# Kernel tuning notes

Measured on AMD Instinct MI355X. Metric: run time of the kernel, lower is better.

## Reference

```python
import jax, jax.numpy as jnp
import numpy as np

EPS = 1e-6
ROPE_BASE = 10000.0


def layer_norm(x, scale, bias):
    mu = jnp.mean(x, axis=-1, keepdims=True)
    var = jnp.mean(jnp.square(x - mu), axis=-1, keepdims=True)
    return (x - mu) * jax.lax.rsqrt(var + EPS) * scale + bias


def make_rope(head_dim, seq_len):
    half = head_dim // 2
    inv_freq = 1.0 / (ROPE_BASE ** (jnp.arange(half, dtype=jnp.float32) / half))
    freqs = jnp.outer(jnp.arange(seq_len, dtype=jnp.float32), inv_freq)  # (T, half)
    cos = jnp.concatenate([jnp.cos(freqs), jnp.cos(freqs)], axis=-1)[:, None, :]  # (T,1,Dh)
    sin = jnp.concatenate([jnp.sin(freqs), jnp.sin(freqs)], axis=-1)[:, None, :]

    def rotate_half(x):
        x1, x2 = x[..., :half], x[..., half:]
        return jnp.concatenate([-x2, x1], axis=-1)

    def apply(q, k):
        return q * cos + rotate_half(q) * sin, k * cos + rotate_half(k) * sin
    return apply


def mha(x, Wq, bq, Wk, bk, Wv, bv, Wo, bo, causal, rope):
    # x: (..., S, D) -> (..., S, D)
    q = jnp.einsum('...sd,dhk->...shk', x, Wq) + bq
    k = jnp.einsum('...sd,dhk->...shk', x, Wk) + bk
    v = jnp.einsum('...sd,dhk->...shk', x, Wv) + bv
    if rope is not None:
        q, k = rope(q, k)
    scale = 1.0 / np.sqrt(q.shape[-1]).astype(np.float32)
    logits = jnp.einsum('...thk,...shk->...hts', q, k) * scale
    if causal:
        S = q.shape[-3]
        mask = jnp.tril(jnp.ones((S, S), dtype=jnp.bool_))
        logits = jnp.where(mask, logits, jnp.finfo(logits.dtype).min)
    probs = jax.nn.softmax(logits, axis=-1)
    o = jnp.einsum('...hts,...shk->...thk', probs, v)
    return jnp.einsum('...thk,hkd->...td', o, Wo) + bo


def setup_inputs() -> dict:
    key = jax.random.key(0)
    B, T, M, D, H, Dh, F = 8, 128, 16, 1024, 16, 64, 4096
    ks = jax.random.split(key, 12)
    s = 0.02
    return {
        'x': jax.random.normal(ks[0], (B, T, M, D), jnp.float32),
        'ln1_scale': jnp.ones((D,), jnp.float32), 'ln1_bias': jnp.zeros((D,), jnp.float32),
        't_Wq': jax.random.normal(ks[1], (D, H, Dh), jnp.float32) * s,
        't_bq': jnp.zeros((H, Dh), jnp.float32),
        't_Wk': jax.random.normal(ks[2], (D, H, Dh), jnp.float32) * s,
        't_bk': jnp.zeros((H, Dh), jnp.float32),
        't_Wv': jax.random.normal(ks[3], (D, H, Dh), jnp.float32) * s,
        't_bv': jnp.zeros((H, Dh), jnp.float32),
        't_Wo': jax.random.normal(ks[4], (H, Dh, D), jnp.float32) * s,
        't_bo': jnp.zeros((D,), jnp.float32),
        'ln2_scale': jnp.ones((D,), jnp.float32), 'ln2_bias': jnp.zeros((D,), jnp.float32),
        'm_Wq': jax.random.normal(ks[5], (D, H, Dh), jnp.float32) * s,
        'm_bq': jnp.zeros((H, Dh), jnp.float32),
        'm_Wk': jax.random.normal(ks[6], (D, H, Dh), jnp.float32) * s,
        'm_bk': jnp.zeros((H, Dh), jnp.float32),
        'm_Wv': jax.random.normal(ks[7], (D, H, Dh), jnp.float32) * s,
        'm_bv': jnp.zeros((H, Dh), jnp.float32),
        'm_Wo': jax.random.normal(ks[8], (H, Dh, D), jnp.float32) * s,
        'm_bo': jnp.zeros((D,), jnp.float32),
        'ln3_scale': jnp.ones((D,), jnp.float32), 'ln3_bias': jnp.zeros((D,), jnp.float32),
        'mlp_W1': jax.random.normal(ks[9], (D, F), jnp.float32) * s,
        'mlp_b1': jnp.zeros((F,), jnp.float32),
        'mlp_W2': jax.random.normal(ks[10], (F, D), jnp.float32) * s,
        'mlp_b2': jnp.zeros((D,), jnp.float32),
    }


def reference(x, ln1_scale, ln1_bias, t_Wq, t_bq, t_Wk, t_bk, t_Wv, t_bv, t_Wo, t_bo,
              ln2_scale, ln2_bias, m_Wq, m_bq, m_Wk, m_bk, m_Wv, m_bv, m_Wo, m_bo,
              ln3_scale, ln3_bias, mlp_W1, mlp_b1, mlp_W2, mlp_b2):
    # x: (B, T, M, D)
    T = x.shape[1]
    Dh = t_Wq.shape[-1]
    rope = make_rope(Dh, T)
    # --- temporal axial attention (causal, RoPE), M folded into batch ---
    h = layer_norm(x, ln1_scale, ln1_bias)
    h = jnp.swapaxes(h, 1, 2)  # (B, M, T, D)
    a = mha(h, t_Wq, t_bq, t_Wk, t_bk, t_Wv, t_bv, t_Wo, t_bo, causal=True, rope=rope)
    x = x + jnp.swapaxes(a, 1, 2)
    # --- modality axial attention (bidirectional, no RoPE), T folded into batch ---
    h = layer_norm(x, ln2_scale, ln2_bias)  # (B, T, M, D), M is seq axis
    x = x + mha(h, m_Wq, m_bq, m_Wk, m_bk, m_Wv, m_bv, m_Wo, m_bo, causal=False, rope=None)
    # --- MLP ---
    h = layer_norm(x, ln3_scale, ln3_bias)
    h = jax.nn.gelu(jnp.einsum('...d,df->...f', h, mlp_W1) + mlp_b1)
    x = x + jnp.einsum('...f,fd->...d', h, mlp_W2) + mlp_b2
    return x
```

## Files before the change

### kernel.cpp

```cpp
#include <hip/hip_runtime.h>
#include <stdint.h>

typedef __attribute__((ext_vector_type(8))) __bf16 bf16x8;
typedef __attribute__((ext_vector_type(4))) float f32x4;

#define DEV static __device__ __forceinline__

DEV unsigned short f2bf(float f) {
    unsigned int u = __float_as_uint(f);
    u = (u + 0x7fffu + ((u >> 16) & 1u)) >> 16;
    return (unsigned short)u;
}
DEV float bf2f(unsigned short h) { return __uint_as_float((unsigned int)h << 16); }

DEV void async_ld16(const void* g, void* l) {
    __builtin_amdgcn_global_load_lds(
        (const __attribute__((address_space(1))) void*)g,
        (__attribute__((address_space(3))) void*)l, 16, 0, 0);
}

DEV f32x4 mfma16(bf16x8 a, bf16x8 b, f32x4 c) {
    return __builtin_amdgcn_mfma_f32_16x16x32_bf16(a, b, c, 0, 0, 0);
}

DEV float gelu_f(float v) {
    float u = 0.7978845608028654f * (v + 0.044715f * v * v * v);
    u = fminf(fmaxf(u, -9.f), 9.f);
    const float e = __expf(2.f * u);
    const float th = (e - 1.f) / (e + 1.f);
    return 0.5f * v * (1.0f + th);
}

__global__ __launch_bounds__(256) void wconv_kernel(
    const float* __restrict__ src, unsigned short* __restrict__ dst, int K, int N)
{
    __shared__ float tile[32][33];
    const int tx = threadIdx.x & 31;
    const int ty = threadIdx.x >> 5;
    const long nb = blockIdx.x;
    const long kb = blockIdx.y;
#pragma unroll
    for (int i = 0; i < 32; i += 8)
        tile[ty + i][tx] = src[(kb * 32 + ty + i) * N + nb * 32 + tx];
    __syncthreads();
#pragma unroll
    for (int i = 0; i < 32; i += 8)
        dst[(nb * 32 + ty + i) * K + kb * 32 + tx] = f2bf(tile[tx][ty + i]);
}

__global__ void pack_bias_kernel(const float* __restrict__ bq, const float* __restrict__ bk,
                                 const float* __restrict__ bv, float* __restrict__ o)
{
    int i = blockIdx.x * 256 + threadIdx.x;
    if (i < 1024) o[i] = bq[i];
    else if (i < 2048) o[i] = bk[i - 1024];
    else if (i < 3072) o[i] = bv[i - 2048];
}

__global__ __launch_bounds__(256) void ln_kernel(
    const float* __restrict__ x, const float* __restrict__ scale,
    const float* __restrict__ bias, unsigned short* __restrict__ out)
{
    const int lane = threadIdx.x & 63;
    const int wave = threadIdx.x >> 6;
    const long tok = (long)blockIdx.x * 4 + wave;
    const float* xp = x + tok * 1024;
    float4 v[4];
    float sum = 0.f, sq = 0.f;
#pragma unroll
    for (int i = 0; i < 4; ++i) {
        v[i] = ((const float4*)xp)[i * 64 + lane];
        sum += v[i].x + v[i].y + v[i].z + v[i].w;
        sq += v[i].x * v[i].x + v[i].y * v[i].y + v[i].z * v[i].z + v[i].w * v[i].w;
    }
#pragma unroll
    for (int off = 1; off < 64; off <<= 1) {
        sum += __shfl_xor(sum, off);
        sq  += __shfl_xor(sq, off);
    }
    const float mu = sum * (1.f / 1024.f);
    const float var = sq * (1.f / 1024.f) - mu * mu;
    const float rs = rsqrtf(var + 1e-6f);
#pragma unroll
    for (int i = 0; i < 4; ++i) {
        const float4 sc = ((const float4*)scale)[i * 64 + lane];
        const float4 bi = ((const float4*)bias)[i * 64 + lane];
        ushort4 o;
        o.x = f2bf((v[i].x - mu) * rs * sc.x + bi.x);
        o.y = f2bf((v[i].y - mu) * rs * sc.y + bi.y);
        o.z = f2bf((v[i].z - mu) * rs * sc.z + bi.z);
        o.w = f2bf((v[i].w - mu) * rs * sc.w + bi.w);
        *(ushort4*)&out[tok * 1024 + (i * 64 + lane) * 4] = o;
    }
}

template <int EPI>
__global__ __launch_bounds__(512, 2) void gemm256_kernel(
    const unsigned short* __restrict__ A, const unsigned short* __restrict__ Bt,
    const float* __restrict__ bias, const float* __restrict__ resid,
    void* __restrict__ Cout, int M, int N, int K, int nbx)
{
    __shared__ __align__(16) unsigned short lds[2][2][16384];
    const int tid = threadIdx.x;
    const int lane = tid & 63;
    const int wave = tid >> 6;
    const int wr = wave >> 2;
    const int wc = wave & 3;
    const int lr = lane & 15;
    const int hi = lane >> 4;

    const int nwg = gridDim.x;
    const int cpx = nwg >> 3;
    int bid = blockIdx.x;
    bid = (bid & 7) * cpx + (bid >> 3);
    const int bx = bid % nbx, by = bid / nbx;
    const long row0 = (long)by * 256;
    const long col0 = (long)bx * 256;

    const int NT = K >> 6;

    const int srow = tid >> 3;
    const int scL = (tid & 7) ^ (srow & 7);
    const unsigned short* gA = A + (row0 + srow) * (long)K + scL * 8;
    const unsigned short* gB = Bt + (col0 + srow) * (long)K + scL * 8;

    auto stage = [&](int kt, int buf) {
        const long ko = (long)kt * 64;
#pragma unroll
        for (int i = 0; i < 4; ++i)
            async_ld16(gA + i * 64 * (long)K + ko, &lds[buf][0][i * 4096 + tid * 8]);
#pragma unroll
        for (int i = 0; i < 4; ++i)
            async_ld16(gB + i * 64 * (long)K + ko, &lds[buf][1][i * 4096 + tid * 8]);
    };

    int cOff[2];
#pragma unroll
    for (int ks = 0; ks < 2; ++ks)
        cOff[ks] = (((ks << 2) | hi) ^ (lr & 7)) << 4;

    f32x4 acc[8][4];
#pragma unroll
    for (int i = 0; i < 8; ++i)
#pragma unroll
        for (int j = 0; j < 4; ++j) acc[i][j] = f32x4{0.f, 0.f, 0.f, 0.f};

    stage(0, 0);
    if (NT > 1) stage(1, 1);

    for (int kt = 0; kt < NT; ++kt) {
        const int cur = kt & 1;
        if (kt == NT - 1) { asm volatile("s_waitcnt vmcnt(0)" ::: "memory"); }
        else              { asm volatile("s_waitcnt vmcnt(8)" ::: "memory"); }
        __builtin_amdgcn_sched_barrier(0);
        __builtin_amdgcn_s_barrier();

        const char* baseA = (const char*)&lds[cur][0][0];
        const char* baseB = (const char*)&lds[cur][1][0];

        bf16x8 bfrag[4][2], afrag[4][2];
#pragma unroll
        for (int n = 0; n < 4; ++n)
#pragma unroll
            for (int ks = 0; ks < 2; ++ks)
                bfrag[n][ks] = *(const bf16x8*)(baseB + (wc * 64 + n * 16 + lr) * 128 + cOff[ks]);
#pragma unroll
        for (int mm = 0; mm < 4; ++mm)
#pragma unroll
            for (int ks = 0; ks < 2; ++ks)
                afrag[mm][ks] = *(const bf16x8*)(baseA + (wr * 128 + mm * 16 + lr) * 128 + cOff[ks]);

        __builtin_amdgcn_s_setprio(1);
#pragma unroll
        for (int ks = 0; ks < 2; ++ks)
#pragma unroll
            for (int mm = 0; mm < 4; ++mm)
#pragma unroll
                for (int n = 0; n < 4; ++n)
                    acc[mm][n] = mfma16(afrag[mm][ks], bfrag[n][ks], acc[mm][n]);
        __builtin_amdgcn_s_setprio(0);

#pragma unroll
        for (int mm = 0; mm < 4; ++mm)
#pragma unroll
            for (int ks = 0; ks < 2; ++ks)
                afrag[mm][ks] = *(const bf16x8*)(baseA + (wr * 128 + 64 + mm * 16 + lr) * 128 + cOff[ks]);

        __builtin_amdgcn_s_setprio(1);
#pragma unroll
        for (int ks = 0; ks < 2; ++ks)
#pragma unroll
            for (int mm = 0; mm < 4; ++mm)
#pragma unroll
                for (int n = 0; n < 4; ++n)
                    acc[4 + mm][n] = mfma16(afrag[mm][ks], bfrag[n][ks], acc[4 + mm][n]);
        __builtin_amdgcn_s_setprio(0);

        __builtin_amdgcn_s_barrier();
        if (kt + 2 < NT) stage(kt + 2, cur);
    }

    float bcol[4];
#pragma unroll
    for (int n = 0; n < 4; ++n) bcol[n] = bias[col0 + wc * 64 + n * 16 + lr];

    if (EPI == 2) {
        float (*eF)[256] = (float (*)[256])&lds[0][0][0];
        float* co = (float*)Cout;
#pragma unroll
        for (int half = 0; half < 2; ++half) {
            if (wr == half) {
#pragma unroll
                for (int m = 0; m < 8; ++m)
#pragma unroll
                    for (int n = 0; n < 4; ++n)
#pragma unroll
                        for (int j = 0; j < 4; ++j)
                            eF[m * 16 + hi * 4 + j][wc * 64 + n * 16 + lr] = acc[m][n][j] + bcol[n];
            }
            __syncthreads();
#pragma unroll
            for (int it = 0; it < 16; ++it) {
                const int idx = it * 512 + tid;
                const int row = idx >> 6;
                const int ch = (idx & 63) * 4;
                const long g = row0 + half * 128 + row;
                float4 v = *(const float4*)&eF[row][ch];
                const float4 rv = *(const float4*)&resid[g * N + col0 + ch];
                v.x += rv.x; v.y += rv.y; v.z += rv.z; v.w += rv.w;
                *(float4*)&co[g * N + col0 + ch] = v;
            }
            __syncthreads();
        }
    } else {
        unsigned short (*eT)[256] = (unsigned short (*)[256])&lds[0][0][0];
        unsigned short* co = (unsigned short*)Cout;
#pragma unroll
        for (int m = 0; m < 8; ++m)
#pragma unroll
            for (int n = 0; n < 4; ++n)
#pragma unroll
                for (int j = 0; j < 4; ++j) {
                    float v = acc[m][n][j] + bcol[n];
                    if (EPI == 1) v = gelu_f(v);
                    eT[wr * 128 + m * 16 + hi * 4 + j][wc * 64 + n * 16 + lr] = f2bf(v);
                }
        __syncthreads();
#pragma unroll
        for (int it = 0; it < 16; ++it) {
            const int idx = it * 512 + tid;
            const int row = idx >> 5;
            const int ch = (idx & 31) * 8;
            *(uint4*)&co[(row0 + row) * N + col0 + ch] = *(const uint4*)&eT[row][ch];
        }
    }
}

__global__ __launch_bounds__(256) void rope_kernel(unsigned short* __restrict__ qkv)
{
    const long tid = (long)blockIdx.x * 256 + threadIdx.x;
    const int d = (int)(tid & 31);
    const int h = (int)((tid >> 5) & 15);
    const int qk = (int)((tid >> 9) & 1);
    const long token = tid >> 10;
    const int t = (int)((token >> 4) & 127);
    unsigned short* p = qkv + token * 3072 + qk * 1024 + h * 64 + d;
    const float x1 = bf2f(p[0]);
    const float x2 = bf2f(p[32]);
    const float inv = __expf((float)d * -0.2878231366242557f);
    const float f = (float)t * inv;
    float sn, cs;
    sincosf(f, &sn, &cs);
    p[0]  = f2bf(x1 * cs - x2 * sn);
    p[32] = f2bf(x2 * cs + x1 * sn);
}

__global__ __launch_bounds__(256) void attn_temporal(
    const unsigned short* __restrict__ qkv, unsigned short* __restrict__ out)
{
    const int bid = blockIdx.x;
    const int h = bid & 15;
    const int mm = (bid >> 4) & 15;
    const int b = bid >> 8;
    const int tid = threadIdx.x;
    const int lane = tid & 63;
    const int wave = tid >> 6;
    const int lr = lane & 15;
    const int lk = (lane >> 4) * 8;
    const int r4 = (lane >> 4) * 4;

    __shared__ __align__(16) unsigned short smemA[128 * 136];
    __shared__ __align__(16) unsigned short smemV[64 * 136];
    unsigned short (*Ks)[72] = (unsigned short (*)[72])smemA;
    unsigned short (*Ps)[136] = (unsigned short (*)[136])smemA;
    unsigned short (*Vt)[136] = (unsigned short (*)[136])smemV;

    const long tokbase = (long)b * 2048 + mm;

#pragma unroll
    for (int i = 0; i < 4; ++i) {
        const int cc = tid + 256 * i;
        const int s = cc >> 3, part = cc & 7;
        const unsigned short* g = qkv + (tokbase + s * 16l) * 3072 + 1024 + h * 64 + part * 8;
        *(uint4*)&Ks[s][part * 8] = *(const uint4*)g;
    }
#pragma unroll
    for (int i = 0; i < 4; ++i) {
        const int cc = tid + 256 * i;
        const int s = cc >> 3, part = cc & 7;
        const unsigned short* g = qkv + (tokbase + s * 16l) * 3072 + 2048 + h * 64 + part * 8;
        union { uint4 u; unsigned short us[8]; } uu;
        uu.u = *(const uint4*)g;
#pragma unroll
        for (int j = 0; j < 8; ++j) Vt[part * 8 + j][s] = uu.us[j];
    }
    __syncthreads();

    bf16x8 qf[2][2];
#pragma unroll
    for (int rb = 0; rb < 2; ++rb)
#pragma unroll
        for (int ks = 0; ks < 2; ++ks) {
            const int t = wave * 32 + rb * 16 + lr;
            qf[rb][ks] = *(const bf16x8*)(qkv + (tokbase + t * 16l) * 3072 + h * 64 + ks * 32 + lk);
        }

    f32x4 sacc[2][8];
#pragma unroll
    for (int rb = 0; rb < 2; ++rb)
#pragma unroll
        for (int cb = 0; cb < 8; ++cb) sacc[rb][cb] = f32x4{0.f, 0.f, 0.f, 0.f};

#pragma unroll
    for (int cb = 0; cb < 8; ++cb)
#pragma unroll
        for (int ks = 0; ks < 2; ++ks) {
            const bf16x8 kf = *(const bf16x8*)&Ks[cb * 16 + lr][ks * 32 + lk];
            sacc[0][cb] = mfma16(qf[0][ks], kf, sacc[0][cb]);
            sacc[1][cb] = mfma16(qf[1][ks], kf, sacc[1][cb]);
        }

    float recip[2][4];
#pragma unroll
    for (int rb = 0; rb < 2; ++rb)
#pragma unroll
        for (int r = 0; r < 4; ++r) {
            const int trow = wave * 32 + rb * 16 + r4 + r;
            float mx = -1e30f;
#pragma unroll
            for (int cb = 0; cb < 8; ++cb) {
                const int s = cb * 16 + lr;
                const float v = (s <= trow) ? sacc[rb][cb][r] * 0.125f : -1e30f;
                sacc[rb][cb][r] = v;
                mx = fmaxf(mx, v);
            }
            mx = fmaxf(mx, __shfl_xor(mx, 1));
            mx = fmaxf(mx, __shfl_xor(mx, 2));
            mx = fmaxf(mx, __shfl_xor(mx, 4));
            mx = fmaxf(mx, __shfl_xor(mx, 8));
            float sum = 0.f;
#pragma unroll
            for (int cb = 0; cb < 8; ++cb) {
                const float e = __expf(sacc[rb][cb][r] - mx);
                sacc[rb][cb][r] = e;
                sum += e;
            }
            sum += __shfl_xor(sum, 1);
            sum += __shfl_xor(sum, 2);
            sum += __shfl_xor(sum, 4);
            sum += __shfl_xor(sum, 8);
            recip[rb][r] = 1.f / sum;
        }
    __syncthreads();

#pragma unroll
    for (int rb = 0; rb < 2; ++rb)
#pragma unroll
        for (int cb = 0; cb < 8; ++cb)
#pragma unroll
            for (int r = 0; r < 4; ++r)
                Ps[wave * 32 + rb * 16 + r4 + r][cb * 16 + lr] = f2bf(sacc[rb][cb][r]);
    __syncthreads();

    f32x4 oacc[2][4];
#pragma unroll
    for (int rb = 0; rb < 2; ++rb)
#pragma unroll
        for (int cb = 0; cb < 4; ++cb) oacc[rb][cb] = f32x4{0.f, 0.f, 0.f, 0.f};

#pragma unroll
    for (int ks = 0; ks < 4; ++ks) {
        bf16x8 pf[2];
        pf[0] = *(const bf16x8*)&Ps[wave * 32 + lr][ks * 32 + lk];
        pf[1] = *(const bf16x8*)&Ps[wave * 32 + 16 + lr][ks * 32 + lk];
#pragma unroll
        for (int cb = 0; cb < 4; ++cb) {
            const bf16x8 vf = *(const bf16x8*)&Vt[cb * 16 + lr][ks * 32 + lk];
            oacc[0][cb] = mfma16(pf[0], vf, oacc[0][cb]);
            oacc[1][cb] = mfma16(pf[1], vf, oacc[1][cb]);
        }
    }

#pragma unroll
    for (int rb = 0; rb < 2; ++rb)
#pragma unroll
        for (int cb = 0; cb < 4; ++cb)
#pragma unroll
            for (int r = 0; r < 4; ++r) {
                const int trow = wave * 32 + rb * 16 + r4 + r;
                out[(tokbase + trow * 16l) * 1024 + h * 64 + cb * 16 + lr] =
                    f2bf(oacc[rb][cb][r] * recip[rb][r]);
            }
}

__global__ __launch_bounds__(256) void attn_modality(
    const unsigned short* __restrict__ qkv, unsigned short* __restrict__ out)
{
    const int tid = threadIdx.x;
    const int lane = tid & 63;
    const int wave = tid >> 6;
    const int lr = lane & 15;
    const int lk = (lane >> 4) * 8;
    const int r4 = (lane >> 4) * 4;
    const long base = (long)blockIdx.x * 16;

    __shared__ __align__(16) unsigned short smem[4][64 * 40 + 16 * 40];
    unsigned short (*Vt)[40] = (unsigned short (*)[40]) & smem[wave][0];
    unsigned short (*Pl)[40] = (unsigned short (*)[40]) & smem[wave][64 * 40];

    for (int i = lane; i < 400; i += 64)
        *(uint4*)&smem[wave][i * 8] = make_uint4(0u, 0u, 0u, 0u);

    for (int hi = 0; hi < 4; ++hi) {
        const int h = wave * 4 + hi;
#pragma unroll
        for (int i = 0; i < 2; ++i) {
            const int cc = lane + 64 * i;
            const int s = cc >> 3, d0 = (cc & 7) * 8;
            union { uint4 u; unsigned short us[8]; } uu;
            uu.u = *(const uint4*)(qkv + (base + s) * 3072 + 2048 + h * 64 + d0);
#pragma unroll
            for (int j = 0; j < 8; ++j) Vt[d0 + j][s] = uu.us[j];
        }
        bf16x8 qf[2], kf[2];
#pragma unroll
        for (int ks = 0; ks < 2; ++ks) {
            qf[ks] = *(const bf16x8*)(qkv + (base + lr) * 3072 + h * 64 + ks * 32 + lk);
            kf[ks] = *(const bf16x8*)(qkv + (base + lr) * 3072 + 1024 + h * 64 + ks * 32 + lk);
        }
        f32x4 sv = f32x4{0.f, 0.f, 0.f, 0.f};
        sv = mfma16(qf[0], kf[0], sv);
        sv = mfma16(qf[1], kf[1], sv);

        float recip[4], pe[4];
#pragma unroll
        for (int r = 0; r < 4; ++r) {
            const float v = sv[r] * 0.125f;
            float mx = v;
            mx = fmaxf(mx, __shfl_xor(mx, 1));
            mx = fmaxf(mx, __shfl_xor(mx, 2));
            mx = fmaxf(mx, __shfl_xor(mx, 4));
            mx = fmaxf(mx, __shfl_xor(mx, 8));
            const float e = __expf(v - mx);
            float sum = e;
            sum += __shfl_xor(sum, 1);
            sum += __shfl_xor(sum, 2);
            sum += __shfl_xor(sum, 4);
            sum += __shfl_xor(sum, 8);
            recip[r] = 1.f / sum;
            pe[r] = e;
        }
#pragma unroll
        for (int r = 0; r < 4; ++r) Pl[r4 + r][lr] = f2bf(pe[r]);

        const bf16x8 pf = *(const bf16x8*)&Pl[lr][lk];
#pragma unroll
        for (int cb = 0; cb < 4; ++cb) {
            const bf16x8 vf = *(const bf16x8*)&Vt[cb * 16 + lr][lk];
            f32x4 o = f32x4{0.f, 0.f, 0.f, 0.f};
            o = mfma16(pf, vf, o);
#pragma unroll
            for (int r = 0; r < 4; ++r)
                out[(base + r4 + r) * 1024 + h * 64 + cb * 16 + lr] = f2bf(o[r] * recip[r]);
        }
    }
}

extern "C" void kernel_launch(void* const* d_in, const int* in_sizes, int n_in,
                              void* d_out, int out_size, void* d_ws, size_t ws_size,
                              hipStream_t stream)
{
    (void)in_sizes; (void)n_in; (void)out_size;
    const float* x    = (const float*)d_in[0];
    const float* ln1s = (const float*)d_in[1];
    const float* ln1b = (const float*)d_in[2];
    const float* tWq  = (const float*)d_in[3];
    const float* tbq  = (const float*)d_in[4];
    const float* tWk  = (const float*)d_in[5];
    const float* tbk  = (const float*)d_in[6];
    const float* tWv  = (const float*)d_in[7];
    const float* tbv  = (const float*)d_in[8];
    const float* tWo  = (const float*)d_in[9];
    const float* tbo  = (const float*)d_in[10];
    const float* ln2s = (const float*)d_in[11];
    const float* ln2b = (const float*)d_in[12];
    const float* mWq  = (const float*)d_in[13];
    const float* mbq  = (const float*)d_in[14];
    const float* mWk  = (const float*)d_in[15];
    const float* mbk  = (const float*)d_in[16];
    const float* mWv  = (const float*)d_in[17];
    const float* mbv  = (const float*)d_in[18];
    const float* mWo  = (const float*)d_in[19];
    const float* mbo  = (const float*)d_in[20];
    const float* ln3s = (const float*)d_in[21];
    const float* ln3b = (const float*)d_in[22];
    const float* W1   = (const float*)d_in[23];
    const float* b1   = (const float*)d_in[24];
    const float* W2   = (const float*)d_in[25];
    const float* b2   = (const float*)d_in[26];

    if (ws_size < 201351168ull) return;

    char* ws = (char*)d_ws;
    unsigned short* Wt_tqkv = (unsigned short*)(ws + 0);
    unsigned short* Wt_to   = (unsigned short*)(ws + 6291456);
    unsigned short* Wt_mqkv = (unsigned short*)(ws + 8388608);
    unsigned short* Wt_mo   = (unsigned short*)(ws + 14680064);
    unsigned short* Wt1     = (unsigned short*)(ws + 16777216);
    unsigned short* Wt2     = (unsigned short*)(ws + 25165824);
    float* bias_t           = (float*)(ws + 33554432);
    float* bias_m           = (float*)(ws + 33566720);
    unsigned short* act     = (unsigned short*)(ws + 33579008);
    unsigned short* qkv     = (unsigned short*)(ws + 67133440);
    unsigned short* hidden  = qkv;
    float* xout = (float*)d_out;

    dim3 blk(256);
    dim3 blk5(512);

    wconv_kernel<<<dim3(32, 32), blk, 0, stream>>>(tWq, Wt_tqkv, 1024, 1024);
    wconv_kernel<<<dim3(32, 32), blk, 0, stream>>>(tWk, Wt_tqkv + 1024 * 1024, 1024, 1024);
    wconv_kernel<<<dim3(32, 32), blk, 0, stream>>>(tWv, Wt_tqkv + 2048 * 1024, 1024, 1024);
    wconv_kernel<<<dim3(32, 32), blk, 0, stream>>>(tWo, Wt_to, 1024, 1024);
    wconv_kernel<<<dim3(32, 32), blk, 0, stream>>>(mWq, Wt_mqkv, 1024, 1024);
    wconv_kernel<<<dim3(32, 32), blk, 0, stream>>>(mWk, Wt_mqkv + 1024 * 1024, 1024, 1024);
    wconv_kernel<<<dim3(32, 32), blk, 0, stream>>>(mWv, Wt_mqkv + 2048 * 1024, 1024, 1024);
    wconv_kernel<<<dim3(32, 32), blk, 0, stream>>>(mWo, Wt_mo, 1024, 1024);
    wconv_kernel<<<dim3(128, 32), blk, 0, stream>>>(W1, Wt1, 1024, 4096);
    wconv_kernel<<<dim3(32, 128), blk, 0, stream>>>(W2, Wt2, 4096, 1024);
    pack_bias_kernel<<<12, blk, 0, stream>>>(tbq, tbk, tbv, bias_t);
    pack_bias_kernel<<<12, blk, 0, stream>>>(mbq, mbk, mbv, bias_m);

    ln_kernel<<<4096, blk, 0, stream>>>(x, ln1s, ln1b, act);
    gemm256_kernel<0><<<768, blk5, 0, stream>>>(act, Wt_tqkv, bias_t, nullptr, qkv, 16384, 3072, 1024, 12);
    rope_kernel<<<65536, blk, 0, stream>>>(qkv);
    attn_temporal<<<2048, blk, 0, stream>>>(qkv, act);
    gemm256_kernel<2><<<256, blk5, 0, stream>>>(act, Wt_to, tbo, x, xout, 16384, 1024, 1024, 4);
    ln_kernel<<<4096, blk, 0, stream>>>(xout, ln2s, ln2b, act);
    gemm256_kernel<0><<<768, blk5, 0, stream>>>(act, Wt_mqkv, bias_m, nullptr, qkv, 16384, 3072, 1024, 12);
    attn_modality<<<1024, blk, 0, stream>>>(qkv, act);
    gemm256_kernel<2><<<256, blk5, 0, stream>>>(act, Wt_mo, mbo, xout, xout, 16384, 1024, 1024, 4);
    ln_kernel<<<4096, blk, 0, stream>>>(xout, ln3s, ln3b, act);
    gemm256_kernel<1><<<1024, blk5, 0, stream>>>(act, Wt1, b1, nullptr, hidden, 16384, 4096, 1024, 16);
    gemm256_kernel<2><<<256, blk5, 0, stream>>>(hidden, Wt2, b2, xout, xout, 16384, 1024, 4096, 4);
}
```

Before: 803.5 us.

## Restructure GEMM into quadrant-pipelined stages and fuse RoPE into QKV epilogue

Splits each K-tile of the GEMM's A and B into halves and interleaves their async loads with four quadrant MFMA phases, each gated by its own waitcnt and barrier, replacing the old two-buffer prefetch. Each wave's output columns are rearranged so that a head's low and high 32-column halves live in the same wave, which lets the temporal QKV GEMM apply RoPE in its epilogue. The standalone rope kernel and its extra read-modify-write pass over q/k are removed. The trade-off is finer-grained synchronisation, with more barriers per K-step, and use of the faster __sincosf intrinsic.

```diff
diff --git a/kernel.cpp b/kernel.cpp
--- a/kernel.cpp
+++ b/kernel.cpp
@@ -94,13 +94,13 @@
     }
 }
 
-template <int EPI>
+template <int EPI, bool ROPE>
 __global__ __launch_bounds__(512, 2) void gemm256_kernel(
     const unsigned short* __restrict__ A, const unsigned short* __restrict__ Bt,
     const float* __restrict__ bias, const float* __restrict__ resid,
     void* __restrict__ Cout, int M, int N, int K, int nbx)
 {
-    __shared__ __align__(16) unsigned short lds[2][2][16384];
+    __shared__ __align__(16) unsigned short lds[2][2][2][8192];
     const int tid = threadIdx.x;
     const int lane = tid & 63;
     const int wave = tid >> 6;
@@ -116,28 +116,37 @@
     const int bx = bid % nbx, by = bid / nbx;
     const long row0 = (long)by * 256;
     const long col0 = (long)bx * 256;
-
     const int NT = K >> 6;
 
-    const int srow = tid >> 3;
-    const int scL = (tid & 7) ^ (srow & 7);
-    const unsigned short* gA = A + (row0 + srow) * (long)K + scL * 8;
-    const unsigned short* gB = Bt + (col0 + srow) * (long)K + scL * 8;
-
-    auto stage = [&](int kt, int buf) {
+    const int tr = tid >> 3;
+    const int gc = (tid & 7) ^ (tr & 7);
+    const unsigned short* srcA = A + (row0 + tr) * (long)K + gc * 8;
+    const unsigned short* srcB = Bt + (col0 + (tr >> 5) * 64 + (tr & 31)) * (long)K + gc * 8;
+
+    auto stageA = [&](int kt, int h) {
         const long ko = (long)kt * 64;
-#pragma unroll
-        for (int i = 0; i < 4; ++i)
-            async_ld16(gA + i * 64 * (long)K + ko, &lds[buf][0][i * 4096 + tid * 8]);
-#pragma unroll
-        for (int i = 0; i < 4; ++i)
-            async_ld16(gB + i * 64 * (long)K + ko, &lds[buf][1][i * 4096 + tid * 8]);
+        unsigned short* dst = &lds[kt & 1][0][h][tid * 8];
+        async_ld16(srcA + (h * 64) * (long)K + ko, dst);
+        async_ld16(srcA + (128 + h * 64) * (long)K + ko, dst + 4096);
     };
-
-    int cOff[2];
-#pragma unroll
-    for (int ks = 0; ks < 2; ++ks)
-        cOff[ks] = (((ks << 2) | hi) ^ (lr & 7)) << 4;
+    auto stageB = [&](int kt, int h) {
+        const long ko = (long)kt * 64;
+        unsigned short* dst = &lds[kt & 1][1][h][tid * 8];
+        async_ld16(srcB + (h * 32) * (long)K + ko, dst);
+        async_ld16(srcB + (128 + h * 32) * (long)K + ko, dst + 4096);
+    };
+
+    int aoff[4][2], boff[2][2];
+#pragma unroll
+    for (int m = 0; m < 4; ++m)
+#pragma unroll
+        for (int ks = 0; ks < 2; ++ks)
+            aoff[m][ks] = (wr * 64 + m * 16 + lr) * 128 + ((((ks * 4) | hi) ^ (lr & 7)) << 4);
+#pragma unroll
+    for (int n = 0; n < 2; ++n)
+#pragma unroll
+        for (int ks = 0; ks < 2; ++ks)
+            boff[n][ks] = (wc * 32 + n * 16 + lr) * 128 + ((((ks * 4) | hi) ^ (lr & 7)) << 4);
 
     f32x4 acc[8][4];
 #pragma unroll
@@ -145,78 +154,109 @@
 #pragma unroll
         for (int j = 0; j < 4; ++j) acc[i][j] = f32x4{0.f, 0.f, 0.f, 0.f};
 
-    stage(0, 0);
-    if (NT > 1) stage(1, 1);
+    stageA(0, 0); stageB(0, 0); stageB(0, 1); stageA(0, 1);
+
+    bf16x8 a[4][2], b0[2][2], b1[2][2];
 
     for (int kt = 0; kt < NT; ++kt) {
-        const int cur = kt & 1;
-        if (kt == NT - 1) { asm volatile("s_waitcnt vmcnt(0)" ::: "memory"); }
-        else              { asm volatile("s_waitcnt vmcnt(8)" ::: "memory"); }
+        const int buf = kt & 1;
+        const bool st = (kt + 1 < NT);
+        const char* bA0 = (const char*)&lds[buf][0][0][0];
+        const char* bA1 = (const char*)&lds[buf][0][1][0];
+        const char* bB0 = (const char*)&lds[buf][1][0][0];
+        const char* bB1 = (const char*)&lds[buf][1][1][0];
+
+        asm volatile("s_waitcnt vmcnt(4)" ::: "memory");
+        __builtin_amdgcn_s_barrier();
         __builtin_amdgcn_sched_barrier(0);
+        if (st) stageA(kt + 1, 0);
+#pragma unroll
+        for (int n = 0; n < 2; ++n)
+#pragma unroll
+            for (int ks = 0; ks < 2; ++ks) b0[n][ks] = *(const bf16x8*)(bB0 + boff[n][ks]);
+#pragma unroll
+        for (int m = 0; m < 4; ++m)
+#pragma unroll
+            for (int ks = 0; ks < 2; ++ks) a[m][ks] = *(const bf16x8*)(bA0 + aoff[m][ks]);
+        __builtin_amdgcn_s_setprio(1);
+#pragma unroll
+        for (int ks = 0; ks < 2; ++ks)
+#pragma unroll
+            for (int m = 0; m < 4; ++m)
+#pragma unroll
+                for (int n = 0; n < 2; ++n)
+                    acc[m][n] = mfma16(a[m][ks], b0[n][ks], acc[m][n]);
+        __builtin_amdgcn_s_setprio(0);
+
+        asm volatile("s_waitcnt vmcnt(4)" ::: "memory");
         __builtin_amdgcn_s_barrier();
-
-        const char* baseA = (const char*)&lds[cur][0][0];
-        const char* baseB = (const char*)&lds[cur][1][0];
-
-        bf16x8 bfrag[4][2], afrag[4][2];
-#pragma unroll
-        for (int n = 0; n < 4; ++n)
-#pragma unroll
-            for (int ks = 0; ks < 2; ++ks)
-                bfrag[n][ks] = *(const bf16x8*)(baseB + (wc * 64 + n * 16 + lr) * 128 + cOff[ks]);
-#pragma unroll
-        for (int mm = 0; mm < 4; ++mm)
-#pragma unroll
-            for (int ks = 0; ks < 2; ++ks)
-                afrag[mm][ks] = *(const bf16x8*)(baseA + (wr * 128 + mm * 16 + lr) * 128 + cOff[ks]);
-
+        __builtin_amdgcn_sched_barrier(0);
+        if (st) stageB(kt + 1, 0);
+#pragma unroll
+        for (int n = 0; n < 2; ++n)
+#pragma unroll
+            for (int ks = 0; ks < 2; ++ks) b1[n][ks] = *(const bf16x8*)(bB1 + boff[n][ks]);
         __builtin_amdgcn_s_setprio(1);
 #pragma unroll
         for (int ks = 0; ks < 2; ++ks)
 #pragma unroll
-            for (int mm = 0; mm < 4; ++mm)
-#pragma unroll
-                for (int n = 0; n < 4; ++n)
-                    acc[mm][n] = mfma16(afrag[mm][ks], bfrag[n][ks], acc[mm][n]);
+            for (int m = 0; m < 4; ++m)
+#pragma unroll
+                for (int n = 0; n < 2; ++n)
+                    acc[m][2 + n] = mfma16(a[m][ks], b1[n][ks], acc[m][2 + n]);
         __builtin_amdgcn_s_setprio(0);
 
-#pragma unroll
-        for (int mm = 0; mm < 4; ++mm)
-#pragma unroll
-            for (int ks = 0; ks < 2; ++ks)
-                afrag[mm][ks] = *(const bf16x8*)(baseA + (wr * 128 + 64 + mm * 16 + lr) * 128 + cOff[ks]);
-
+        asm volatile("s_waitcnt vmcnt(4)" ::: "memory");
+        __builtin_amdgcn_s_barrier();
+        __builtin_amdgcn_sched_barrier(0);
+        if (st) stageB(kt + 1, 1);
+#pragma unroll
+        for (int m = 0; m < 4; ++m)
+#pragma unroll
+            for (int ks = 0; ks < 2; ++ks) a[m][ks] = *(const bf16x8*)(bA1 + aoff[m][ks]);
         __builtin_amdgcn_s_setprio(1);
 #pragma unroll
         for (int ks = 0; ks < 2; ++ks)
 #pragma unroll
-            for (int mm = 0; mm < 4; ++mm)
-#pragma unroll
-                for (int n = 0; n < 4; ++n)
-                    acc[4 + mm][n] = mfma16(afrag[mm][ks], bfrag[n][ks], acc[4 + mm][n]);
+            for (int m = 0; m < 4; ++m)
+#pragma unroll
+                for (int n = 0; n < 2; ++n)
+                    acc[4 + m][n] = mfma16(a[m][ks], b0[n][ks], acc[4 + m][n]);
         __builtin_amdgcn_s_setprio(0);
 
-        __builtin_amdgcn_s_barrier();
-        if (kt + 2 < NT) stage(kt + 2, cur);
-    }
+        if (st) stageA(kt + 1, 1);
+        __builtin_amdgcn_s_setprio(1);
+#pragma unroll
+        for (int ks = 0; ks < 2; ++ks)
+#pragma unroll
+            for (int m = 0; m < 4; ++m)
+#pragma unroll
+                for (int n = 0; n < 2; ++n)
+                    acc[4 + m][2 + n] = mfma16(a[m][ks], b1[n][ks], acc[4 + m][2 + n]);
+        __builtin_amdgcn_s_setprio(0);
+    }
+
+    __syncthreads();
 
     float bcol[4];
 #pragma unroll
-    for (int n = 0; n < 4; ++n) bcol[n] = bias[col0 + wc * 64 + n * 16 + lr];
+    for (int cn = 0; cn < 4; ++cn)
+        bcol[cn] = bias[col0 + wc * 64 + (cn >> 1) * 32 + (cn & 1) * 16 + lr];
 
     if (EPI == 2) {
-        float (*eF)[256] = (float (*)[256])&lds[0][0][0];
+        float (*eF)[256] = (float (*)[256])&lds[0][0][0][0];
         float* co = (float*)Cout;
 #pragma unroll
         for (int half = 0; half < 2; ++half) {
             if (wr == half) {
 #pragma unroll
-                for (int m = 0; m < 8; ++m)
-#pragma unroll
-                    for (int n = 0; n < 4; ++n)
+                for (int i = 0; i < 8; ++i)
+#pragma unroll
+                    for (int cn = 0; cn < 4; ++cn)
 #pragma unroll
                         for (int j = 0; j < 4; ++j)
-                            eF[m * 16 + hi * 4 + j][wc * 64 + n * 16 + lr] = acc[m][n][j] + bcol[n];
+                            eF[(i >> 2) * 64 + (i & 3) * 16 + hi * 4 + j]
+                              [wc * 64 + (cn >> 1) * 32 + (cn & 1) * 16 + lr] = acc[i][cn][j] + bcol[cn];
             }
             __syncthreads();
 #pragma unroll
@@ -233,18 +273,42 @@
             __syncthreads();
         }
     } else {
-        unsigned short (*eT)[256] = (unsigned short (*)[256])&lds[0][0][0];
+        unsigned short (*eT)[256] = (unsigned short (*)[256])&lds[0][0][0][0];
         unsigned short* co = (unsigned short*)Cout;
-#pragma unroll
-        for (int m = 0; m < 8; ++m)
-#pragma unroll
-            for (int n = 0; n < 4; ++n)
-#pragma unroll
-                for (int j = 0; j < 4; ++j) {
-                    float v = acc[m][n][j] + bcol[n];
-                    if (EPI == 1) v = gelu_f(v);
-                    eT[wr * 128 + m * 16 + hi * 4 + j][wc * 64 + n * 16 + lr] = f2bf(v);
+        const bool doRope = ROPE && (col0 + wc * 64) < 2048;
+        if (doRope) {
+#pragma unroll
+            for (int i = 0; i < 8; ++i) {
+                const int rbase = (i >> 2) * 64 + (i & 3) * 16;
+                const float t_i = (float)(int)(((row0 + wr * 128 + rbase) >> 4) & 127);
+#pragma unroll
+                for (int cn = 0; cn < 2; ++cn) {
+                    const float dd = (float)(cn * 16 + lr);
+                    const float inv = __expf(dd * -0.2878231366242557f);
+                    float sn, cs;
+                    __sincosf(t_i * inv, &sn, &cs);
+#pragma unroll
+                    for (int j = 0; j < 4; ++j) {
+                        const float lo = acc[i][cn][j] + bcol[cn];
+                        const float hv = acc[i][cn + 2][j] + bcol[cn + 2];
+                        eT[wr * 128 + rbase + hi * 4 + j][wc * 64 + cn * 16 + lr] = f2bf(lo * cs - hv * sn);
+                        eT[wr * 128 + rbase + hi * 4 + j][wc * 64 + 32 + cn * 16 + lr] = f2bf(hv * cs + lo * sn);
+                    }
                 }
+            }
+        } else {
+#pragma unroll
+            for (int i = 0; i < 8; ++i)
+#pragma unroll
+                for (int cn = 0; cn < 4; ++cn)
+#pragma unroll
+                    for (int j = 0; j < 4; ++j) {
+                        float v = acc[i][cn][j] + bcol[cn];
+                        if (EPI == 1) v = gelu_f(v);
+                        eT[wr * 128 + (i >> 2) * 64 + (i & 3) * 16 + hi * 4 + j]
+                          [wc * 64 + (cn >> 1) * 32 + (cn & 1) * 16 + lr] = f2bf(v);
+                    }
+        }
         __syncthreads();
 #pragma unroll
         for (int it = 0; it < 16; ++it) {
@@ -254,25 +318,6 @@
             *(uint4*)&co[(row0 + row) * N + col0 + ch] = *(const uint4*)&eT[row][ch];
         }
     }
-}
-
-__global__ __launch_bounds__(256) void rope_kernel(unsigned short* __restrict__ qkv)
-{
-    const long tid = (long)blockIdx.x * 256 + threadIdx.x;
-    const int d = (int)(tid & 31);
-    const int h = (int)((tid >> 5) & 15);
-    const int qk = (int)((tid >> 9) & 1);
-    const long token = tid >> 10;
-    const int t = (int)((token >> 4) & 127);
-    unsigned short* p = qkv + token * 3072 + qk * 1024 + h * 64 + d;
-    const float x1 = bf2f(p[0]);
-    const float x2 = bf2f(p[32]);
-    const float inv = __expf((float)d * -0.2878231366242557f);
-    const float f = (float)t * inv;
-    float sn, cs;
-    sincosf(f, &sn, &cs);
-    p[0]  = f2bf(x1 * cs - x2 * sn);
-    p[32] = f2bf(x2 * cs + x1 * sn);
 }
 
 __global__ __launch_bounds__(256) void attn_temporal(
@@ -552,15 +597,14 @@
     pack_bias_kernel<<<12, blk, 0, stream>>>(mbq, mbk, mbv, bias_m);
 
     ln_kernel<<<4096, blk, 0, stream>>>(x, ln1s, ln1b, act);
-    gemm256_kernel<0><<<768, blk5, 0, stream>>>(act, Wt_tqkv, bias_t, nullptr, qkv, 16384, 3072, 1024, 12);
-    rope_kernel<<<65536, blk, 0, stream>>>(qkv);
+    gemm256_kernel<0, true><<<768, blk5, 0, stream>>>(act, Wt_tqkv, bias_t, nullptr, qkv, 16384, 3072, 1024, 12);
     attn_temporal<<<2048, blk, 0, stream>>>(qkv, act);
-    gemm256_kernel<2><<<256, blk5, 0, stream>>>(act, Wt_to, tbo, x, xout, 16384, 1024, 1024, 4);
+    gemm256_kernel<2, false><<<256, blk5, 0, stream>>>(act, Wt_to, tbo, x, xout, 16384, 1024, 1024, 4);
     ln_kernel<<<4096, blk, 0, stream>>>(xout, ln2s, ln2b, act);
-    gemm256_kernel<0><<<768, blk5, 0, stream>>>(act, Wt_mqkv, bias_m, nullptr, qkv, 16384, 3072, 1024, 12);
+    gemm256_kernel<0, false><<<768, blk5, 0, stream>>>(act, Wt_mqkv, bias_m, nullptr, qkv, 16384, 3072, 1024, 12);
     attn_modality<<<1024, blk, 0, stream>>>(qkv, act);
-    gemm256_kernel<2><<<256, blk5, 0, stream>>>(act, Wt_mo, mbo, xout, xout, 16384, 1024, 1024, 4);
+    gemm256_kernel<2, false><<<256, blk5, 0, stream>>>(act, Wt_mo, mbo, xout, xout, 16384, 1024, 1024, 4);
     ln_kernel<<<4096, blk, 0, stream>>>(xout, ln3s, ln3b, act);
-    gemm256_kernel<1><<<1024, blk5, 0, stream>>>(act, Wt1, b1, nullptr, hidden, 16384, 4096, 1024, 16);
-    gemm256_kernel<2><<<256, blk5, 0, stream>>>(hidden, Wt2, b2, xout, xout, 16384, 1024, 4096, 4);
-}
+    gemm256_kernel<1, false><<<1024, blk5, 0, stream>>>(act, Wt1, b1, nullptr, hidden, 16384, 4096, 1024, 16);
+    gemm256_kernel<2, false><<<256, blk5, 0, stream>>>(hidden, Wt2, b2, xout, xout, 16384, 1024, 4096, 4);
+}
```

Measured after the change: 755.9 us. -5.9%, faster.

## Triple-buffer GEMM with K=32 tiles and fuse RoPE into QKV epilogue

Applied to the files above, without the earlier changes.

The GEMM mainloop now uses 32-wide K tiles with a three-slot LDS ring and issues the next-but-one prefetch right after the barrier, so global loads overlap the MFMA work with only one barrier-protected wait per step. The LDS footprint shrinks (3x2x8192 halves instead of 2x2x16384), and epilogues are split into halves or quarters to fit the smaller buffer. RoPE is fused into the temporal QKV GEMM epilogue, which removes the standalone rope_kernel pass over qkv. The cost is more loop iterations and barriers per K, plus fast __sincosf in place of sincosf.

```diff
diff --git a/kernel.cpp b/kernel.cpp
--- a/kernel.cpp
+++ b/kernel.cpp
@@ -94,13 +94,13 @@
     }
 }
 
-template <int EPI>
+template <int EPI, bool ROPE>
 __global__ __launch_bounds__(512, 2) void gemm256_kernel(
     const unsigned short* __restrict__ A, const unsigned short* __restrict__ Bt,
     const float* __restrict__ bias, const float* __restrict__ resid,
     void* __restrict__ Cout, int M, int N, int K, int nbx)
 {
-    __shared__ __align__(16) unsigned short lds[2][2][16384];
+    __shared__ __align__(16) unsigned short lds[3][2][8192];
     const int tid = threadIdx.x;
     const int lane = tid & 63;
     const int wave = tid >> 6;
@@ -116,28 +116,35 @@
     const int bx = bid % nbx, by = bid / nbx;
     const long row0 = (long)by * 256;
     const long col0 = (long)bx * 256;
-
-    const int NT = K >> 6;
-
-    const int srow = tid >> 3;
-    const int scL = (tid & 7) ^ (srow & 7);
-    const unsigned short* gA = A + (row0 + srow) * (long)K + scL * 8;
-    const unsigned short* gB = Bt + (col0 + srow) * (long)K + scL * 8;
-
-    auto stage = [&](int kt, int buf) {
-        const long ko = (long)kt * 64;
-#pragma unroll
-        for (int i = 0; i < 4; ++i)
-            async_ld16(gA + i * 64 * (long)K + ko, &lds[buf][0][i * 4096 + tid * 8]);
-#pragma unroll
-        for (int i = 0; i < 4; ++i)
-            async_ld16(gB + i * 64 * (long)K + ko, &lds[buf][1][i * 4096 + tid * 8]);
+    const int NT = K >> 5;
+
+    const int r_ = tid >> 2;
+    const int pc = tid & 3;
+    const int sxr = (r_ >> 1) & 3;
+    const unsigned short* gA0 = A + (row0 + r_) * (long)K + (pc ^ sxr) * 8;
+    const unsigned short* gA1 = A + (row0 + r_ + 128) * (long)K + (pc ^ sxr) * 8;
+    const unsigned short* gB0 = Bt + (col0 + r_) * (long)K + (pc ^ sxr) * 8;
+    const unsigned short* gB1 = Bt + (col0 + r_ + 128) * (long)K + (pc ^ sxr) * 8;
+
+    auto stage = [&](int buf, int kt) {
+        const long ko = (long)kt * 32;
+        async_ld16(gA0 + ko, &lds[buf][0][tid * 8]);
+        async_ld16(gA1 + ko, &lds[buf][0][tid * 8 + 4096]);
+        async_ld16(gB0 + ko, &lds[buf][1][tid * 8]);
+        async_ld16(gB1 + ko, &lds[buf][1][tid * 8 + 4096]);
     };
 
-    int cOff[2];
-#pragma unroll
-    for (int ks = 0; ks < 2; ++ks)
-        cOff[ks] = (((ks << 2) | hi) ^ (lr & 7)) << 4;
+    int aoff[8], boff[4];
+#pragma unroll
+    for (int m = 0; m < 8; ++m) {
+        const int row = wr * 128 + m * 16 + lr;
+        aoff[m] = row * 64 + ((hi ^ ((row >> 1) & 3)) << 4);
+    }
+#pragma unroll
+    for (int n = 0; n < 4; ++n) {
+        const int row = wc * 64 + n * 16 + lr;
+        boff[n] = row * 64 + ((hi ^ ((row >> 1) & 3)) << 4);
+    }
 
     f32x4 acc[8][4];
 #pragma unroll
@@ -146,59 +153,44 @@
         for (int j = 0; j < 4; ++j) acc[i][j] = f32x4{0.f, 0.f, 0.f, 0.f};
 
     stage(0, 0);
-    if (NT > 1) stage(1, 1);
+    stage(1, 1);
+    int cur = 0, sb = 2;
 
     for (int kt = 0; kt < NT; ++kt) {
-        const int cur = kt & 1;
-        if (kt == NT - 1) { asm volatile("s_waitcnt vmcnt(0)" ::: "memory"); }
-        else              { asm volatile("s_waitcnt vmcnt(8)" ::: "memory"); }
+        __builtin_amdgcn_sched_barrier(0);
+        if (kt + 1 < NT) { asm volatile("s_waitcnt vmcnt(4)" ::: "memory"); }
+        else             { asm volatile("s_waitcnt vmcnt(0)" ::: "memory"); }
         __builtin_amdgcn_sched_barrier(0);
         __builtin_amdgcn_s_barrier();
-
-        const char* baseA = (const char*)&lds[cur][0][0];
-        const char* baseB = (const char*)&lds[cur][1][0];
-
-        bf16x8 bfrag[4][2], afrag[4][2];
-#pragma unroll
-        for (int n = 0; n < 4; ++n)
-#pragma unroll
-            for (int ks = 0; ks < 2; ++ks)
-                bfrag[n][ks] = *(const bf16x8*)(baseB + (wc * 64 + n * 16 + lr) * 128 + cOff[ks]);
-#pragma unroll
-        for (int mm = 0; mm < 4; ++mm)
-#pragma unroll
-            for (int ks = 0; ks < 2; ++ks)
-                afrag[mm][ks] = *(const bf16x8*)(baseA + (wr * 128 + mm * 16 + lr) * 128 + cOff[ks]);
+        __builtin_amdgcn_sched_barrier(0);
+
+        if (kt + 2 < NT) stage(sb, kt + 2);
+        __builtin_amdgcn_sched_barrier(0);
+
+        const char* bA = (const char*)&lds[cur][0][0];
+        const char* bB = (const char*)&lds[cur][1][0];
+        bf16x8 a[8], b[4];
+#pragma unroll
+        for (int n = 0; n < 4; ++n) b[n] = *(const bf16x8*)(bB + boff[n]);
+#pragma unroll
+        for (int m = 0; m < 8; ++m) a[m] = *(const bf16x8*)(bA + aoff[m]);
 
         __builtin_amdgcn_s_setprio(1);
 #pragma unroll
-        for (int ks = 0; ks < 2; ++ks)
-#pragma unroll
-            for (int mm = 0; mm < 4; ++mm)
-#pragma unroll
-                for (int n = 0; n < 4; ++n)
-                    acc[mm][n] = mfma16(afrag[mm][ks], bfrag[n][ks], acc[mm][n]);
+        for (int m = 0; m < 8; ++m)
+#pragma unroll
+            for (int n = 0; n < 4; ++n)
+                acc[m][n] = mfma16(a[m], b[n], acc[m][n]);
         __builtin_amdgcn_s_setprio(0);
 
-#pragma unroll
-        for (int mm = 0; mm < 4; ++mm)
-#pragma unroll
-            for (int ks = 0; ks < 2; ++ks)
-                afrag[mm][ks] = *(const bf16x8*)(baseA + (wr * 128 + 64 + mm * 16 + lr) * 128 + cOff[ks]);
-
-        __builtin_amdgcn_s_setprio(1);
-#pragma unroll
-        for (int ks = 0; ks < 2; ++ks)
-#pragma unroll
-            for (int mm = 0; mm < 4; ++mm)
-#pragma unroll
-                for (int n = 0; n < 4; ++n)
-                    acc[4 + mm][n] = mfma16(afrag[mm][ks], bfrag[n][ks], acc[4 + mm][n]);
-        __builtin_amdgcn_s_setprio(0);
-
+        __builtin_amdgcn_sched_barrier(0);
         __builtin_amdgcn_s_barrier();
-        if (kt + 2 < NT) stage(kt + 2, cur);
-    }
+        __builtin_amdgcn_sched_barrier(0);
+        cur = (cur == 2) ? 0 : cur + 1;
+        sb = (sb == 2) ? 0 : sb + 1;
+    }
+
+    __syncthreads();
 
     float bcol[4];
 #pragma unroll
@@ -208,23 +200,25 @@
         float (*eF)[256] = (float (*)[256])&lds[0][0][0];
         float* co = (float*)Cout;
 #pragma unroll
-        for (int half = 0; half < 2; ++half) {
-            if (wr == half) {
-#pragma unroll
-                for (int m = 0; m < 8; ++m)
+        for (int q = 0; q < 4; ++q) {
+            if (wr == (q >> 1)) {
+                const int ib = (q & 1) * 4;
+#pragma unroll
+                for (int k2 = 0; k2 < 4; ++k2)
 #pragma unroll
                     for (int n = 0; n < 4; ++n)
 #pragma unroll
                         for (int j = 0; j < 4; ++j)
-                            eF[m * 16 + hi * 4 + j][wc * 64 + n * 16 + lr] = acc[m][n][j] + bcol[n];
+                            eF[k2 * 16 + hi * 4 + j][wc * 64 + n * 16 + lr] =
+                                acc[ib + k2][n][j] + bcol[n];
             }
             __syncthreads();
 #pragma unroll
-            for (int it = 0; it < 16; ++it) {
+            for (int it = 0; it < 8; ++it) {
                 const int idx = it * 512 + tid;
                 const int row = idx >> 6;
                 const int ch = (idx & 63) * 4;
-                const long g = row0 + half * 128 + row;
+                const long g = row0 + q * 64 + row;
                 float4 v = *(const float4*)&eF[row][ch];
                 const float4 rv = *(const float4*)&resid[g * N + col0 + ch];
                 v.x += rv.x; v.y += rv.y; v.z += rv.z; v.w += rv.w;
@@ -235,44 +229,53 @@
     } else {
         unsigned short (*eT)[256] = (unsigned short (*)[256])&lds[0][0][0];
         unsigned short* co = (unsigned short*)Cout;
-#pragma unroll
-        for (int m = 0; m < 8; ++m)
-#pragma unroll
-            for (int n = 0; n < 4; ++n)
-#pragma unroll
-                for (int j = 0; j < 4; ++j) {
-                    float v = acc[m][n][j] + bcol[n];
-                    if (EPI == 1) v = gelu_f(v);
-                    eT[wr * 128 + m * 16 + hi * 4 + j][wc * 64 + n * 16 + lr] = f2bf(v);
+        const bool doRope = ROPE && (col0 + wc * 64) < 2048;
+#pragma unroll
+        for (int h2 = 0; h2 < 2; ++h2) {
+            if (wr == h2) {
+                if (doRope) {
+#pragma unroll
+                    for (int i = 0; i < 8; ++i) {
+                        const float t_i = (float)(int)(((row0 + h2 * 128 + i * 16) >> 4) & 127);
+#pragma unroll
+                        for (int n = 0; n < 2; ++n) {
+                            const float dd = (float)(n * 16 + lr);
+                            const float inv = __expf(dd * -0.2878231366242557f);
+                            float sn, cs;
+                            __sincosf(t_i * inv, &sn, &cs);
+#pragma unroll
+                            for (int j = 0; j < 4; ++j) {
+                                const float lo = acc[i][n][j] + bcol[n];
+                                const float hv = acc[i][n + 2][j] + bcol[n + 2];
+                                eT[i * 16 + hi * 4 + j][wc * 64 + n * 16 + lr] = f2bf(lo * cs - hv * sn);
+                                eT[i * 16 + hi * 4 + j][wc * 64 + 32 + n * 16 + lr] = f2bf(hv * cs + lo * sn);
+                            }
+                        }
+                    }
+                } else {
+#pragma unroll
+                    for (int i = 0; i < 8; ++i)
+#pragma unroll
+                        for (int n = 0; n < 4; ++n)
+#pragma unroll
+                            for (int j = 0; j < 4; ++j) {
+                                float v = acc[i][n][j] + bcol[n];
+                                if (EPI == 1) v = gelu_f(v);
+                                eT[i * 16 + hi * 4 + j][wc * 64 + n * 16 + lr] = f2bf(v);
+                            }
                 }
-        __syncthreads();
-#pragma unroll
-        for (int it = 0; it < 16; ++it) {
-            const int idx = it * 512 + tid;
-            const int row = idx >> 5;
-            const int ch = (idx & 31) * 8;
-            *(uint4*)&co[(row0 + row) * N + col0 + ch] = *(const uint4*)&eT[row][ch];
-        }
-    }
-}
-
-__global__ __launch_bounds__(256) void rope_kernel(unsigned short* __restrict__ qkv)
-{
-    const long tid = (long)blockIdx.x * 256 + threadIdx.x;
-    const int d = (int)(tid & 31);
-    const int h = (int)((tid >> 5) & 15);
-    const int qk = (int)((tid >> 9) & 1);
-    const long token = tid >> 10;
-    const int t = (int)((token >> 4) & 127);
-    unsigned short* p = qkv + token * 3072 + qk * 1024 + h * 64 + d;
-    const float x1 = bf2f(p[0]);
-    const float x2 = bf2f(p[32]);
-    const float inv = __expf((float)d * -0.2878231366242557f);
-    const float f = (float)t * inv;
-    float sn, cs;
-    sincosf(f, &sn, &cs);
-    p[0]  = f2bf(x1 * cs - x2 * sn);
-    p[32] = f2bf(x2 * cs + x1 * sn);
+            }
+            __syncthreads();
+#pragma unroll
+            for (int it = 0; it < 8; ++it) {
+                const int idx = it * 512 + tid;
+                const int row = idx >> 5;
+                const int ch = (idx & 31) * 8;
+                *(uint4*)&co[(row0 + h2 * 128 + row) * N + col0 + ch] = *(const uint4*)&eT[row][ch];
+            }
+            __syncthreads();
+        }
+    }
 }
 
 __global__ __launch_bounds__(256) void attn_temporal(
@@ -552,15 +555,14 @@
     pack_bias_kernel<<<12, blk, 0, stream>>>(mbq, mbk, mbv, bias_m);
 
     ln_kernel<<<4096, blk, 0, stream>>>(x, ln1s, ln1b, act);
-    gemm256_kernel<0><<<768, blk5, 0, stream>>>(act, Wt_tqkv, bias_t, nullptr, qkv, 16384, 3072, 1024, 12);
-    rope_kernel<<<65536, blk, 0, stream>>>(qkv);
+    gemm256_kernel<0, true><<<768, blk5, 0, stream>>>(act, Wt_tqkv, bias_t, nullptr, qkv, 16384, 3072, 1024, 12);
     attn_temporal<<<2048, blk, 0, stream>>>(qkv, act);
-    gemm256_kernel<2><<<256, blk5, 0, stream>>>(act, Wt_to, tbo, x, xout, 16384, 1024, 1024, 4);
+    gemm256_kernel<2, false><<<256, blk5, 0, stream>>>(act, Wt_to, tbo, x, xout, 16384, 1024, 1024, 4);
     ln_kernel<<<4096, blk, 0, stream>>>(xout, ln2s, ln2b, act);
-    gemm256_kernel<0><<<768, blk5, 0, stream>>>(act, Wt_mqkv, bias_m, nullptr, qkv, 16384, 3072, 1024, 12);
+    gemm256_kernel<0, false><<<768, blk5, 0, stream>>>(act, Wt_mqkv, bias_m, nullptr, qkv, 16384, 3072, 1024, 12);
     attn_modality<<<1024, blk, 0, stream>>>(qkv, act);
-    gemm256_kernel<2><<<256, blk5, 0, stream>>>(act, Wt_mo, mbo, xout, xout, 16384, 1024, 1024, 4);
+    gemm256_kernel<2, false><<<256, blk5, 0, stream>>>(act, Wt_mo, mbo, xout, xout, 16384, 1024, 1024, 4);
     ln_kernel<<<4096, blk, 0, stream>>>(xout, ln3s, ln3b, act);
-    gemm256_kernel<1><<<1024, blk5, 0, stream>>>(act, Wt1, b1, nullptr, hidden, 16384, 4096, 1024, 16);
-    gemm256_kernel<2><<<256, blk5, 0, stream>>>(hidden, Wt2, b2, xout, xout, 16384, 1024, 4096, 4);
-}
+    gemm256_kernel<1, false><<<1024, blk5, 0, stream>>>(act, Wt1, b1, nullptr, hidden, 16384, 4096, 1024, 16);
+    gemm256_kernel<2, false><<<256, blk5, 0, stream>>>(hidden, Wt2, b2, xout, xout, 16384, 1024, 4096, 4);
+}
```

Result: slower. 825.6 us (+2.8%).
